# Kernel optimization log

Measured on AMD Instinct MI355X. Metric: run time of the kernel, lower is better.

## Reference

```python
import jax, jax.numpy as jnp
import numpy as np

# Model dims (match init_kwargs)
D_MODEL, D_STATE, D_CONV, EXPAND = 256, 16, 4, 2
D_INNER = EXPAND * D_MODEL           # 512
DT_RANK = (D_MODEL + 15) // 16       # 16
NS_SMALL, NS_BIG = 64, 16
N_BRANCH = 6                         # fwd, bwd, small-slice fwd/bwd, big-slice fwd/bwd
BATCH, SEQLEN = 2, 2048


def setup_inputs() -> dict:
    key = jax.random.key(0)
    ks = jax.random.split(key, 12)
    R2N = DT_RANK + 2 * D_STATE
    # dt_proj bias init as in the module: inverse-softplus of dt ~ LogUniform[1e-3, 1e-1]
    dt = jnp.exp(jax.random.uniform(ks[0], (N_BRANCH, D_INNER)) * (np.log(0.1) - np.log(0.001)) + np.log(0.001))
    dt = jnp.clip(dt, 1e-4, None)
    dt_b = dt + jnp.log(-jnp.expm1(-dt))
    A_log = jnp.log(jnp.broadcast_to(jnp.arange(1, D_STATE + 1, dtype=jnp.float32), (N_BRANCH, D_INNER, D_STATE)))
    return {
        "hidden_states": jax.random.normal(ks[1], (BATCH, SEQLEN, D_MODEL), jnp.float32),
        "in_w": jax.random.normal(ks[2], (2 * D_INNER, D_MODEL), jnp.float32) * (D_MODEL ** -0.5),
        "out_w": jax.random.normal(ks[3], (D_MODEL, D_INNER), jnp.float32) * (D_INNER ** -0.5),
        "conv_w": jax.random.normal(ks[4], (N_BRANCH, D_INNER, D_CONV), jnp.float32) * (D_CONV ** -0.5),
        "conv_b": jax.random.normal(ks[5], (N_BRANCH, D_INNER), jnp.float32) * 0.02,
        "xproj_w": jax.random.normal(ks[6], (N_BRANCH, R2N, D_INNER), jnp.float32) * (D_INNER ** -0.5),
        "dt_w": jax.random.uniform(ks[7], (N_BRANCH, D_INNER, DT_RANK), jnp.float32, -(DT_RANK ** -0.5), DT_RANK ** -0.5),
        "dt_b": dt_b.astype(jnp.float32),
        "A_log": A_log,
        "D_skip": jnp.ones((N_BRANCH, D_INNER), jnp.float32),
    }


def _causal_dwconv(x, w, b):
    # x: (B, D, L); w: (D, K); b: (D,). Causal depthwise conv (torch padding=K-1, keep first L).
    K = w.shape[-1]
    L = x.shape[-1]
    xp = jnp.pad(x, ((0, 0), (0, 0), (K - 1, 0)))
    y = sum(w[:, k][None, :, None] * xp[:, :, k:k + L] for k in range(K))
    return y + b[None, :, None]


def _ssm_scan(delta, u, Bm, Cm, A):
    # delta, u: (B, D, L); Bm, Cm: (B, N, L); A: (D, N) negative reals.
    dT = jnp.moveaxis(delta, -1, 0)  # (L, B, D)
    uT = jnp.moveaxis(u, -1, 0)
    BT = jnp.moveaxis(Bm, -1, 0)     # (L, B, N)
    CT = jnp.moveaxis(Cm, -1, 0)

    def step(h, inp):
        d_t, u_t, b_t, c_t = inp
        dA = jnp.exp(d_t[..., None] * A)                       # (B, D, N)
        h = dA * h + (d_t * u_t)[..., None] * b_t[:, None, :]  # (B, D, N)
        y = jnp.einsum('bdn,bn->bd', h, c_t)
        return h, y

    h0 = jnp.zeros(delta.shape[:2] + (A.shape[-1],), delta.dtype)
    _, ys = jax.lax.scan(step, h0, (dT, uT, BT, CT))
    return jnp.moveaxis(ys, 0, -1)  # (B, D, L)


def _slice_interleave(xz, ns):
    # torch: chunk(ns, dim=-1) -> stack(dim=-1) -> flatten(-2)
    B_, D_, L_ = xz.shape
    return xz.reshape(B_, D_, ns, L_ // ns).swapaxes(-1, -2).reshape(B_, D_, L_)


def _slice_restore(y, ns):
    # torch: reshape(B, D, L//ns, ns).permute(0,1,3,2).flatten(-2)
    B_, D_, L_ = y.shape
    return y.reshape(B_, D_, L_ // ns, ns).swapaxes(-1, -2).reshape(B_, D_, L_)


def reference(hidden_states, in_w, out_w, conv_w, conv_b, xproj_w, dt_w, dt_b, A_log, D_skip):
    R, N = DT_RANK, D_STATE
    xz = jnp.einsum('bld,ed->bel', hidden_states, in_w)  # (B, 2*d_inner, L)

    def branch(xz_i, i):
        x, z = jnp.split(xz_i, 2, axis=1)
        u = jax.nn.silu(_causal_dwconv(x, conv_w[i], conv_b[i]))
        x_dbl = jnp.einsum('bdl,rd->brl', u, xproj_w[i])       # (B, R+2N, L)
        dt_low, Bm, Cm = x_dbl[:, :R], x_dbl[:, R:R + N], x_dbl[:, R + N:]
        delta = jax.nn.softplus(jnp.einsum('brl,dr->bdl', dt_low, dt_w[i]) + dt_b[i][None, :, None])
        A = -jnp.exp(A_log[i])
        y = _ssm_scan(delta, u, Bm, Cm, A) + u * D_skip[i][None, :, None]
        return y * jax.nn.silu(z)

    out = branch(xz, 0)
    out_b = jnp.flip(branch(jnp.flip(xz, -1), 1), -1)
    xz_s = _slice_interleave(xz, NS_SMALL)
    out_s = _slice_restore(branch(xz_s, 2), NS_SMALL)
    out_s_b = _slice_restore(branch(jnp.flip(xz_s, -1), 3), NS_SMALL)
    xz_big = _slice_interleave(xz, NS_BIG)
    out_big = _slice_restore(branch(xz_big, 4), NS_BIG)
    out_big_b = _slice_restore(branch(jnp.flip(xz_big, -1), 5), NS_BIG)

    total = out + out_b + out_s + out_s_b + out_big + out_big_b  # (B, d_inner, L)
    return jnp.einsum('bdl,od->blo', total, out_w)               # (B, L, d_model)
```

## Files before the change

### kernel.cpp

```cpp
#include <hip/hip_runtime.h>
#include <hip/hip_bf16.h>

#define SEQ 2048

typedef __hip_bfloat16 bf16;

__device__ __forceinline__ float silu_f(float x){ return x / (1.f + __expf(-x)); }

__global__ __launch_bounds__(256) void k_ingemm2(const float* __restrict__ hid,
                                                 const float* __restrict__ in_w,
                                                 float* __restrict__ xz,
                                                 const float* __restrict__ xw,
                                                 float* __restrict__ xwT){
    __shared__ float tile[64][65];
    int bid = blockIdx.x;
    if (bid >= 1024) {
        int t = (bid - 1024) * 256 + (int)threadIdx.x;
        int r = t % 48; int dd = (t / 48) % 512; int i = t / (48 * 512);
        xwT[t] = xw[(i * 48 + r) * 512 + dd];
        return;
    }
    int lblk = bid & 31; int eblk = (bid >> 5) & 15; int b = bid >> 9;
    int lane = threadIdx.x & 63;
    int ew = __builtin_amdgcn_readfirstlane((int)threadIdx.x >> 6);
    int l = lblk * 64 + lane;
    int e0 = eblk * 64 + ew * 16;
    int row = threadIdx.x >> 2;
    int c0  = (threadIdx.x & 3) * 16;
    float acc[16];
    #pragma unroll
    for (int k = 0; k < 16; ++k) acc[k] = 0.f;
    for (int dblk = 0; dblk < 4; ++dblk) {
        __syncthreads();
        const float* src = hid + ((size_t)(b * 2048 + lblk * 64 + row)) * 256 + dblk * 64 + c0;
        float4 v0 = *(const float4*)(src + 0);
        float4 v1 = *(const float4*)(src + 4);
        float4 v2 = *(const float4*)(src + 8);
        float4 v3 = *(const float4*)(src + 12);
        tile[row][c0+ 0]=v0.x; tile[row][c0+ 1]=v0.y; tile[row][c0+ 2]=v0.z; tile[row][c0+ 3]=v0.w;
        tile[row][c0+ 4]=v1.x; tile[row][c0+ 5]=v1.y; tile[row][c0+ 6]=v1.z; tile[row][c0+ 7]=v1.w;
        tile[row][c0+ 8]=v2.x; tile[row][c0+ 9]=v2.y; tile[row][c0+10]=v2.z; tile[row][c0+11]=v2.w;
        tile[row][c0+12]=v3.x; tile[row][c0+13]=v3.y; tile[row][c0+14]=v3.z; tile[row][c0+15]=v3.w;
        __syncthreads();
        for (int dd = 0; dd < 64; ++dd) {
            float hv = tile[lane][dd];
            int dg = dblk * 64 + dd;
            #pragma unroll
            for (int k = 0; k < 16; ++k)
                acc[k] = fmaf(in_w[(e0 + k) * 256 + dg], hv, acc[k]);
        }
    }
    #pragma unroll
    for (int k = 0; k < 16; ++k)
        xz[((size_t)(b * 1024 + e0 + k)) * SEQ + l] = acc[k];
}

__global__ __launch_bounds__(256) void k_conv3(const float* __restrict__ xz,
                                               const float* __restrict__ conv_w,
                                               const float* __restrict__ conv_b,
                                               float* __restrict__ u){
    __shared__ float xs[2112];
    int bid = blockIdx.x;
    int d = bid & 511; int b = (bid >> 9) & 1; int p = bid >> 10;
    int sh = (p == 0) ? 11 : (p == 1) ? 6 : 4;
    int mul = SEQ >> sh;
    int inv = 11 - sh;
    const float* xrow = xz + ((size_t)(b * 1024 + d)) * SEQ;
    #pragma unroll
    for (int k = 0; k < 8; ++k) {
        int l = (int)threadIdx.x + k * 256;
        float v = xrow[l];
        int jj = ((l & (mul - 1)) << sh) | (l >> inv);
        xs[jj + (jj >> 5)] = v;
    }
    __syncthreads();
    #pragma unroll
    for (int f = 0; f < 2; ++f) {
        int i = 2 * p + f;
        float w0 = conv_w[(i * 512 + d) * 4 + 0];
        float w1 = conv_w[(i * 512 + d) * 4 + 1];
        float w2 = conv_w[(i * 512 + d) * 4 + 2];
        float w3 = conv_w[(i * 512 + d) * 4 + 3];
        float cb = conv_b[i * 512 + d];
        float* urow = u + ((size_t)((i * 2 + b) * 512 + d)) * SEQ;
        #pragma unroll
        for (int k = 0; k < 8; ++k) {
            int j = (int)threadIdx.x + k * 256;
            float acc = cb;
            #pragma unroll
            for (int m = 0; m < 4; ++m) {
                int idx = j - 3 + m;
                float xv = 0.f;
                if (idx >= 0) {
                    int ridx = f ? (2047 - idx) : idx;
                    xv = xs[ridx + (ridx >> 5)];
                }
                float wm = (m == 0) ? w0 : (m == 1) ? w1 : (m == 2) ? w2 : w3;
                acc = fmaf(wm, xv, acc);
            }
            urow[j] = silu_f(acc);
        }
    }
}

__global__ __launch_bounds__(256) void k_xproj2(const float* __restrict__ u,
                                                const float* __restrict__ xwT,
                                                float* __restrict__ xpart){
    int bid = blockIdx.x;
    int ib = bid % 12; int jt = (bid / 12) % 8; int dq = bid / 96;
    int j = jt * 256 + (int)threadIdx.x;
    int i = ib >> 1;
    const float* ub = u + ((size_t)ib * 512 + dq * 64) * SEQ + j;
    const float* wb = xwT + ((size_t)i * 512 + dq * 64) * 48;
    float acc[48];
    #pragma unroll
    for (int r = 0; r < 48; ++r) acc[r] = 0.f;
    for (int dd = 0; dd < 64; ++dd) {
        float uv = ub[dd * SEQ];
        const float* w = wb + dd * 48;
        #pragma unroll
        for (int r = 0; r < 48; ++r)
            acc[r] = fmaf(w[r], uv, acc[r]);
    }
    float* op = xpart + ((size_t)(dq * 12 + ib) * 48) * SEQ + j;
    #pragma unroll
    for (int r = 0; r < 48; ++r) op[r * SEQ] = acc[r];
}

__global__ __launch_bounds__(256) void k_xbt(const float* __restrict__ xpart,
                                             float* __restrict__ dtlowb,
                                             float* __restrict__ btJ){
    int t = blockIdx.x * 256 + threadIdx.x;
    const int STR = 12 * 48 * SEQ;
    float s = ((xpart[t]           + xpart[t + STR])     + (xpart[t + 2*STR] + xpart[t + 3*STR]))
            + ((xpart[t + 4*STR]   + xpart[t + 5*STR])   + (xpart[t + 6*STR] + xpart[t + 7*STR]));
    int j = t & 2047; int r = (t >> 11) % 48; int ib = t / (48 * 2048);
    if (r < 16) {
        dtlowb[((size_t)(ib * 16 + r)) * 2048 + j] = s;
    } else {
        int q = r - 16; int bc = q >> 4; int n = q & 15; int n2 = n & 3; int k = n >> 2;
        int tt = j & 31; int cc = j >> 5;
        btJ[(((size_t)(ib * 32 + tt) * 64 + cc) << 5) + bc * 16 + n2 * 4 + k] = s;
    }
}

__global__ __launch_bounds__(256, 8) void k_scan(float* __restrict__ u,
                                                 const float* __restrict__ dtlowb,
                                                 const float* __restrict__ btJ,
                                                 const float* __restrict__ dt_w,
                                                 const float* __restrict__ dt_b,
                                                 const float* __restrict__ D_skip){
    __shared__ float sdel[2304];
    __shared__ bf16 sdu[2304];
    __shared__ float sh[1024];
    __shared__ float sS[64];
    int w = blockIdx.x;
    int tid = threadIdx.x;
    int cc = tid >> 2;
    int n2 = tid & 3;
    int d = w & 511; int ib = w >> 9; int i = ib >> 1;
    float Dd = D_skip[i * 512 + d];
    bool s0 = ((n2 + 1) & 1) != 0;
    bool s1 = ((n2 + 1) & 2) != 0;
    bool s2 = ((n2 + 1) & 4) != 0;

    const float4* wv4 = (const float4*)(dt_w + ((size_t)(i * 512 + d)) * 16);
    float4 dw0 = wv4[0], dw1 = wv4[1], dw2 = wv4[2], dw3 = wv4[3];
    float dtb = dt_b[i * 512 + d];

    float4* ug4 = (float4*)(u + (size_t)w * SEQ);
    float4* sd4 = (float4*)sdel;
    __hip_bfloat162* sdu2 = (__hip_bfloat162*)sdu;
    const float4* dtl4 = (const float4*)(dtlowb + (size_t)ib * 16 * 2048);

    float4 ureg0, ureg1;
    #pragma unroll
    for (int part = 0; part < 2; ++part) {
        int jf = tid + part * 256;
        float4 uu = ug4[jf];
        if (part == 0) ureg0 = uu; else ureg1 = uu;
        float4 acc = make_float4(dtb, dtb, dtb, dtb);
        #pragma unroll
        for (int r = 0; r < 16; ++r) {
            float wr = (r < 4)  ? ((r & 3) == 0 ? dw0.x : (r & 3) == 1 ? dw0.y : (r & 3) == 2 ? dw0.z : dw0.w)
                     : (r < 8)  ? ((r & 3) == 0 ? dw1.x : (r & 3) == 1 ? dw1.y : (r & 3) == 2 ? dw1.z : dw1.w)
                     : (r < 12) ? ((r & 3) == 0 ? dw2.x : (r & 3) == 1 ? dw2.y : (r & 3) == 2 ? dw2.z : dw2.w)
                                : ((r & 3) == 0 ? dw3.x : (r & 3) == 1 ? dw3.y : (r & 3) == 2 ? dw3.z : dw3.w);
            float4 q = dtl4[r * 512 + jf];
            acc.x = fmaf(wr, q.x, acc.x);
            acc.y = fmaf(wr, q.y, acc.y);
            acc.z = fmaf(wr, q.z, acc.z);
            acc.w = fmaf(wr, q.w, acc.w);
        }
        float4 Ev, duv;
        {
            float sp = fmaxf(acc.x, 0.f) + __logf(1.f + __expf(-fabsf(acc.x)));
            Ev.x = __expf(-sp); duv.x = sp * uu.x;
            sp = fmaxf(acc.y, 0.f) + __logf(1.f + __expf(-fabsf(acc.y)));
            Ev.y = __expf(-sp); duv.y = sp * uu.y;
            sp = fmaxf(acc.z, 0.f) + __logf(1.f + __expf(-fabsf(acc.z)));
            Ev.z = __expf(-sp); duv.z = sp * uu.z;
            sp = fmaxf(acc.w, 0.f) + __logf(1.f + __expf(-fabsf(acc.w)));
            Ev.w = __expf(-sp); duv.w = sp * uu.w;
        }
        sd4[jf + (jf >> 3)] = Ev;
        int eb = 2 * (jf + (jf >> 3));
        __hip_bfloat162 p0; p0.x = __float2bfloat16(duv.x); p0.y = __float2bfloat16(duv.y);
        __hip_bfloat162 p1; p1.x = __float2bfloat16(duv.z); p1.y = __float2bfloat16(duv.w);
        sdu2[eb]     = p0;
        sdu2[eb + 1] = p1;
    }
    __syncthreads();

    int cbase = cc * 36;
    const float4* bp4 = (const float4*)btJ + ((size_t)ib * 32 * 64 * 8) + cc * 8 + n2;

    float h0 = 0.f, h1 = 0.f, h2 = 0.f, h3 = 0.f, P = 1.f;
    #pragma unroll 4
    for (int tt = 0; tt < 32; ++tt) {
        float E  = sdel[cbase + tt];
        float du = __bfloat162float(sdu[cbase + tt]);
        float4 B = bp4[tt * 512];
        float E2 = E * E, E4 = E2 * E2;
        float e = (s0 ? E : 1.f) * (s1 ? E2 : 1.f) * (s2 ? E4 : 1.f);
        h0 = fmaf(e, h0, du * B.x); e *= E4;
        h1 = fmaf(e, h1, du * B.y); e *= E4;
        h2 = fmaf(e, h2, du * B.z); e *= E4;
        h3 = fmaf(e, h3, du * B.w);
        P *= E;
    }
    sh[cc * 16 + n2]      = h0;
    sh[cc * 16 + n2 + 4]  = h1;
    sh[cc * 16 + n2 + 8]  = h2;
    sh[cc * 16 + n2 + 12] = h3;
    if (n2 == 0) sS[cc] = P;
    __syncthreads();

    if (tid < 16) {
        float hh = 0.f;
        #pragma unroll 4
        for (int c = 0; c < 64; ++c) {
            float Es = sS[c];
            int e = tid + 1;
            float r = 1.f, bsq = Es;
            #pragma unroll
            for (int bit = 0; bit < 5; ++bit) { if (e & 1) r *= bsq; bsq *= bsq; e >>= 1; }
            float tmp = sh[c * 16 + tid];
            sh[c * 16 + tid] = hh;
            hh = fmaf(r, hh, tmp);
        }
    }
    __syncthreads();

    h0 = sh[cc * 16 + n2];
    h1 = sh[cc * 16 + n2 + 4];
    h2 = sh[cc * 16 + n2 + 8];
    h3 = sh[cc * 16 + n2 + 12];
    #pragma unroll 4
    for (int tt = 0; tt < 32; ++tt) {
        float E  = sdel[cbase + tt];
        float du = __bfloat162float(sdu[cbase + tt]);
        float4 B = bp4[tt * 512];
        float4 C = bp4[tt * 512 + 4];
        float E2 = E * E, E4 = E2 * E2;
        float e = (s0 ? E : 1.f) * (s1 ? E2 : 1.f) * (s2 ? E4 : 1.f);
        h0 = fmaf(e, h0, du * B.x); e *= E4;
        h1 = fmaf(e, h1, du * B.y); e *= E4;
        h2 = fmaf(e, h2, du * B.z); e *= E4;
        h3 = fmaf(e, h3, du * B.w);
        float p = h0 * C.x;
        p = fmaf(h1, C.y, p);
        p = fmaf(h2, C.z, p);
        p = fmaf(h3, C.w, p);
        p += __shfl_xor(p, 1, 4);
        p += __shfl_xor(p, 2, 4);
        if (n2 == 0) sdel[cbase + tt] = p;
    }
    __syncthreads();

    {
        int jf = tid;
        float4 y = sd4[jf + (jf >> 3)];
        y.x = fmaf(ureg0.x, Dd, y.x); y.y = fmaf(ureg0.y, Dd, y.y);
        y.z = fmaf(ureg0.z, Dd, y.z); y.w = fmaf(ureg0.w, Dd, y.w);
        ug4[jf] = y;
        jf = tid + 256;
        y = sd4[jf + (jf >> 3)];
        y.x = fmaf(ureg1.x, Dd, y.x); y.y = fmaf(ureg1.y, Dd, y.y);
        y.z = fmaf(ureg1.z, Dd, y.z); y.w = fmaf(ureg1.w, Dd, y.w);
        ug4[jf] = y;
    }
}

__global__ __launch_bounds__(256) void k_gather(const float* __restrict__ y,
                                                const float* __restrict__ xz,
                                                float* __restrict__ total){
    __shared__ bf16 s2[2112], s3[2112], s4[2112], s5[2112];
    int bid = blockIdx.x;
    int d = bid & 511; int b = bid >> 9;
    long base = (long)(b * 512 + d) * SEQ;
    const float* y0 = y + (0 * 1024) * SEQ + base;
    const float* y1 = y + (1 * 1024) * SEQ + base;
    const float* y2r = y + (2 * 1024) * SEQ + base;
    const float* y3r = y + (3 * 1024) * SEQ + base;
    const float* y4r = y + (4 * 1024) * SEQ + base;
    const float* y5r = y + (5 * 1024) * SEQ + base;
    #pragma unroll
    for (int k = 0; k < 8; ++k) {
        int j = (int)threadIdx.x + k * 256;
        int a = j + (j >> 5);
        s2[a] = __float2bfloat16(y2r[j]);
        s3[a] = __float2bfloat16(y3r[j]);
        s4[a] = __float2bfloat16(y4r[j]);
        s5[a] = __float2bfloat16(y5r[j]);
    }
    __syncthreads();
    const float* zrow = xz + (b * 1024 + 512 + d) * SEQ;
    float* trow = total + (b * 512 + d) * SEQ;
    #pragma unroll
    for (int k = 0; k < 8; ++k) {
        int l = (int)threadIdx.x + k * 256;
        int j2 = ((l & 31) << 6) | (l >> 5);
        int j4 = ((l & 127) << 4) | (l >> 7);
        int a2 = j2 + (j2 >> 5);
        int a4 = j4 + (j4 >> 5);
        float s_fwd = y0[l] + y1[2047 - l] + __bfloat162float(s2[a2]) + __bfloat162float(s4[a4]);
        float s_bwd = __bfloat162float(s3[a2]) + __bfloat162float(s5[a4]);
        float zl = silu_f(zrow[l]);
        float zr = silu_f(zrow[2047 - l]);
        trow[l] = fmaf(s_fwd, zl, s_bwd * zr);
    }
}

__global__ __launch_bounds__(256) void k_outgemm(const float* __restrict__ total,
                                                 const float* __restrict__ out_w,
                                                 float* __restrict__ out){
    int lane = threadIdx.x & 63;
    int ow = __builtin_amdgcn_readfirstlane((int)threadIdx.x >> 6);
    int bid = blockIdx.x;
    int lblk = bid & 31; int oblk = (bid >> 5) & 15; int b = bid >> 9;
    int l = lblk * 64 + lane;
    int o0 = oblk * 16 + ow * 4;
    const float* trow = total + b * 512 * SEQ + l;
    float acc[4] = {0,0,0,0};
    for (int d = 0; d < 512; d += 4) {
        float t0 = trow[(d + 0) * SEQ];
        float t1 = trow[(d + 1) * SEQ];
        float t2 = trow[(d + 2) * SEQ];
        float t3 = trow[(d + 3) * SEQ];
        #pragma unroll
        for (int k = 0; k < 4; ++k) {
            float4 wv = *(const float4*)(out_w + (o0 + k) * 512 + d);
            acc[k] = fmaf(wv.x, t0, fmaf(wv.y, t1, fmaf(wv.z, t2, fmaf(wv.w, t3, acc[k]))));
        }
    }
    float* orow = out + ((long)(b * 2048 + l)) * 256 + o0;
    #pragma unroll
    for (int k = 0; k < 4; ++k) orow[k] = acc[k];
}

extern "C" void kernel_launch(void* const* d_in, const int* in_sizes, int n_in,
                              void* d_out, int out_size, void* d_ws, size_t ws_size,
                              hipStream_t stream) {
    const float* hid    = (const float*)d_in[0];
    const float* in_w   = (const float*)d_in[1];
    const float* out_w  = (const float*)d_in[2];
    const float* conv_w = (const float*)d_in[3];
    const float* conv_b = (const float*)d_in[4];
    const float* xw     = (const float*)d_in[5];
    const float* dt_w   = (const float*)d_in[6];
    const float* dt_b   = (const float*)d_in[7];
    const float* D_skip = (const float*)d_in[9];
    float* out = (float*)d_out;

    const size_t off_xz    = 0;
    const size_t off_u     = 4194304;
    const size_t off_xpart = 16777216;
    const size_t off_total = 30539776;
    const size_t need = (size_t)32636928 * 4;
    if (ws_size < need) return;

    float* xz    = (float*)d_ws + off_xz;
    float* u     = (float*)d_ws + off_u;
    float* xpart = (float*)d_ws + off_xpart;
    float* total = (float*)d_ws + off_total;
    float* btJ    = total;
    float* xwT    = total + 786432;
    float* dtlowb = total + 933888;

    k_ingemm2 <<<1600, 256, 0, stream>>>(hid, in_w, xz, xw, xwT);
    k_conv3   <<<3072, 256, 0, stream>>>(xz, conv_w, conv_b, u);
    k_xproj2  <<<768,  256, 0, stream>>>(u, xwT, xpart);
    k_xbt     <<<4608, 256, 0, stream>>>(xpart, dtlowb, btJ);
    k_scan    <<<6144, 256, 0, stream>>>(u, dtlowb, btJ, dt_w, dt_b, D_skip);
    k_gather  <<<1024, 256, 0, stream>>>(u, xz, total);
    k_outgemm <<<1024, 256, 0, stream>>>(total, out_w, out);
}
```

Measured before the change: 384.4 us.

## Fuse x-projection split-K reduction into projection kernel and restructure chunked scan

Merges the x-projection and its separate split-K reduction kernel into one kernel that reduces partial sums in shared memory and writes dt_low and the B/C layout directly. This removes the large xpart round trip through global memory and one launch. The scan is reorganised into 128 chunks of 16 steps with 8 states per thread, a two-level parallel carry propagation and a new B/C layout, with occupancy hint lowered to 7. Only 384 blocks now run the projection, so parallelism there drops.

Result: slower. 754.0 us (+96.1%).

```diff
diff --git a/kernel.cpp b/kernel.cpp
--- a/kernel.cpp
+++ b/kernel.cpp
@@ -103,73 +103,87 @@
     }
 }
 
-__global__ __launch_bounds__(256) void k_xproj2(const float* __restrict__ u,
+__global__ __launch_bounds__(256) void k_xproj3(const float* __restrict__ u,
                                                 const float* __restrict__ xwT,
-                                                float* __restrict__ xpart){
+                                                float* __restrict__ dtlowb,
+                                                float* __restrict__ btJ){
+    __shared__ __align__(16) float sred[12288];
     int bid = blockIdx.x;
-    int ib = bid % 12; int jt = (bid / 12) % 8; int dq = bid / 96;
-    int j = jt * 256 + (int)threadIdx.x;
-    int i = ib >> 1;
-    const float* ub = u + ((size_t)ib * 512 + dq * 64) * SEQ + j;
-    const float* wb = xwT + ((size_t)i * 512 + dq * 64) * 48;
+    int jt = bid & 31; int ib = bid >> 5; int i = ib >> 1;
+    int tid = (int)threadIdx.x;
+    int j = tid & 63;
+    int ks = __builtin_amdgcn_readfirstlane(tid >> 6);
+    int j0 = jt * 64;
+    const float* ub = u + ((size_t)(ib * 512 + ks * 128)) * SEQ + j0 + j;
+    const float* wb = xwT + ((size_t)(i * 512 + ks * 128)) * 48;
     float acc[48];
     #pragma unroll
     for (int r = 0; r < 48; ++r) acc[r] = 0.f;
-    for (int dd = 0; dd < 64; ++dd) {
-        float uv = ub[dd * SEQ];
-        const float* w = wb + dd * 48;
-        #pragma unroll
-        for (int r = 0; r < 48; ++r)
-            acc[r] = fmaf(w[r], uv, acc[r]);
-    }
-    float* op = xpart + ((size_t)(dq * 12 + ib) * 48) * SEQ + j;
-    #pragma unroll
-    for (int r = 0; r < 48; ++r) op[r * SEQ] = acc[r];
-}
-
-__global__ __launch_bounds__(256) void k_xbt(const float* __restrict__ xpart,
-                                             float* __restrict__ dtlowb,
-                                             float* __restrict__ btJ){
-    int t = blockIdx.x * 256 + threadIdx.x;
-    const int STR = 12 * 48 * SEQ;
-    float s = ((xpart[t]           + xpart[t + STR])     + (xpart[t + 2*STR] + xpart[t + 3*STR]))
-            + ((xpart[t + 4*STR]   + xpart[t + 5*STR])   + (xpart[t + 6*STR] + xpart[t + 7*STR]));
-    int j = t & 2047; int r = (t >> 11) % 48; int ib = t / (48 * 2048);
-    if (r < 16) {
-        dtlowb[((size_t)(ib * 16 + r)) * 2048 + j] = s;
-    } else {
-        int q = r - 16; int bc = q >> 4; int n = q & 15; int n2 = n & 3; int k = n >> 2;
-        int tt = j & 31; int cc = j >> 5;
-        btJ[(((size_t)(ib * 32 + tt) * 64 + cc) << 5) + bc * 16 + n2 * 4 + k] = s;
-    }
-}
-
-__global__ __launch_bounds__(256, 8) void k_scan(float* __restrict__ u,
+    #pragma unroll 4
+    for (int dd = 0; dd < 128; ++dd) {
+        float uv = ub[(size_t)dd * SEQ];
+        const float* ww = wb + dd * 48;
+        #pragma unroll
+        for (int r = 0; r < 48; ++r) acc[r] = fmaf(ww[r], uv, acc[r]);
+    }
+    #pragma unroll
+    for (int r = 0; r < 48; ++r) sred[r * 256 + tid] = acc[r];
+    __syncthreads();
+    const float4* sred4 = (const float4*)sred;
+    {
+        int rr = tid >> 4; int j4 = tid & 15;
+        float4 a0 = sred4[rr * 64 +  0 + j4];
+        float4 a1 = sred4[rr * 64 + 16 + j4];
+        float4 a2 = sred4[rr * 64 + 32 + j4];
+        float4 a3 = sred4[rr * 64 + 48 + j4];
+        float4 s;
+        s.x = (a0.x + a1.x) + (a2.x + a3.x);
+        s.y = (a0.y + a1.y) + (a2.y + a3.y);
+        s.z = (a0.z + a1.z) + (a2.z + a3.z);
+        s.w = (a0.w + a1.w) + (a2.w + a3.w);
+        ((float4*)(dtlowb + ((size_t)(ib * 16 + rr)) * SEQ + j0))[j4] = s;
+    }
+    {
+        int sel = tid >> 5; int n2 = sel & 1; int mq = (sel >> 1) & 1; int bc = sel >> 2;
+        int jb = tid & 31;
+        #pragma unroll
+        for (int half = 0; half < 2; ++half) {
+            int jj = jb + half * 32;
+            int jg = j0 + jj; int cc = jg >> 4; int tt = jg & 15;
+            float4 v;
+            #pragma unroll
+            for (int mm = 0; mm < 4; ++mm) {
+                int row = 16 + bc * 16 + n2 + 8 * mq + 2 * mm;
+                const float* rp = sred + row * 256 + jj;
+                float s = (rp[0] + rp[64]) + (rp[128] + rp[192]);
+                (&v.x)[mm] = s;
+            }
+            ((float4*)btJ)[((((size_t)(ib * 128 + cc) * 2 + n2) * 2 + bc) * 2 + mq) * 16 + tt] = v;
+        }
+    }
+}
+
+__global__ __launch_bounds__(256, 7) void k_scan(float* __restrict__ u,
                                                  const float* __restrict__ dtlowb,
                                                  const float* __restrict__ btJ,
                                                  const float* __restrict__ dt_w,
                                                  const float* __restrict__ dt_b,
                                                  const float* __restrict__ D_skip){
-    __shared__ float sdel[2304];
-    __shared__ bf16 sdu[2304];
-    __shared__ float sh[1024];
-    __shared__ float sS[64];
+    __shared__ __align__(16) float sdel[2560];
+    __shared__ __align__(16) bf16  sdu[2048];
+    __shared__ __align__(16) float shh[2048];
+    __shared__ float sS[128];
     int w = blockIdx.x;
-    int tid = threadIdx.x;
-    int cc = tid >> 2;
-    int n2 = tid & 3;
+    int tid = (int)threadIdx.x;
     int d = w & 511; int ib = w >> 9; int i = ib >> 1;
     float Dd = D_skip[i * 512 + d];
-    bool s0 = ((n2 + 1) & 1) != 0;
-    bool s1 = ((n2 + 1) & 2) != 0;
-    bool s2 = ((n2 + 1) & 4) != 0;
 
     const float4* wv4 = (const float4*)(dt_w + ((size_t)(i * 512 + d)) * 16);
     float4 dw0 = wv4[0], dw1 = wv4[1], dw2 = wv4[2], dw3 = wv4[3];
     float dtb = dt_b[i * 512 + d];
 
     float4* ug4 = (float4*)(u + (size_t)w * SEQ);
-    float4* sd4 = (float4*)sdel;
+    float4* sdel4 = (float4*)sdel;
     __hip_bfloat162* sdu2 = (__hip_bfloat162*)sdu;
     const float4* dtl4 = (const float4*)(dtlowb + (size_t)ib * 16 * 2048);
 
@@ -203,92 +217,145 @@
             sp = fmaxf(acc.w, 0.f) + __logf(1.f + __expf(-fabsf(acc.w)));
             Ev.w = __expf(-sp); duv.w = sp * uu.w;
         }
-        sd4[jf + (jf >> 3)] = Ev;
-        int eb = 2 * (jf + (jf >> 3));
+        int ccw = jf >> 2; int tq = jf & 3;
+        sdel4[ccw * 5 + tq] = Ev;
         __hip_bfloat162 p0; p0.x = __float2bfloat16(duv.x); p0.y = __float2bfloat16(duv.y);
         __hip_bfloat162 p1; p1.x = __float2bfloat16(duv.z); p1.y = __float2bfloat16(duv.w);
-        sdu2[eb]     = p0;
-        sdu2[eb + 1] = p1;
-    }
-    __syncthreads();
-
-    int cbase = cc * 36;
-    const float4* bp4 = (const float4*)btJ + ((size_t)ib * 32 * 64 * 8) + cc * 8 + n2;
-
-    float h0 = 0.f, h1 = 0.f, h2 = 0.f, h3 = 0.f, P = 1.f;
-    #pragma unroll 4
-    for (int tt = 0; tt < 32; ++tt) {
-        float E  = sdel[cbase + tt];
-        float du = __bfloat162float(sdu[cbase + tt]);
-        float4 B = bp4[tt * 512];
-        float E2 = E * E, E4 = E2 * E2;
-        float e = (s0 ? E : 1.f) * (s1 ? E2 : 1.f) * (s2 ? E4 : 1.f);
-        h0 = fmaf(e, h0, du * B.x); e *= E4;
-        h1 = fmaf(e, h1, du * B.y); e *= E4;
-        h2 = fmaf(e, h2, du * B.z); e *= E4;
-        h3 = fmaf(e, h3, du * B.w);
-        P *= E;
-    }
-    sh[cc * 16 + n2]      = h0;
-    sh[cc * 16 + n2 + 4]  = h1;
-    sh[cc * 16 + n2 + 8]  = h2;
-    sh[cc * 16 + n2 + 12] = h3;
-    if (n2 == 0) sS[cc] = P;
-    __syncthreads();
-
-    if (tid < 16) {
-        float hh = 0.f;
-        #pragma unroll 4
-        for (int c = 0; c < 64; ++c) {
-            float Es = sS[c];
-            int e = tid + 1;
-            float r = 1.f, bsq = Es;
+        sdu2[ccw * 8 + tq * 2]     = p0;
+        sdu2[ccw * 8 + tq * 2 + 1] = p1;
+    }
+    __syncthreads();
+
+    int cc = tid >> 1; int n2 = tid & 1;
+    const float4* bt4 = (const float4*)btJ + ((size_t)((ib * 128 + cc) * 2 + n2)) * 64;
+    const uint2* sduq = (const uint2*)sdu;
+
+    float h0=0.f,h1=0.f,h2=0.f,h3=0.f,h4=0.f,h5=0.f,h6=0.f,h7=0.f;
+    float P = 1.f;
+    #pragma unroll
+    for (int tg = 0; tg < 4; ++tg) {
+        float4 Ev = sdel4[cc * 5 + tg];
+        uint2 dz = sduq[cc * 4 + tg];
+        #pragma unroll
+        for (int q = 0; q < 4; ++q) {
+            int tt = tg * 4 + q;
+            float E = (&Ev.x)[q];
+            unsigned ubits = (q < 2) ? dz.x : dz.y;
+            float du = __uint_as_float((q & 1) ? (ubits & 0xffff0000u) : (ubits << 16));
+            float4 B0 = bt4[tt];
+            float4 B1 = bt4[16 + tt];
+            float E2 = E * E;
+            float e = n2 ? E2 : E;
+            h0 = fmaf(e, h0, du * B0.x); e *= E2;
+            h1 = fmaf(e, h1, du * B0.y); e *= E2;
+            h2 = fmaf(e, h2, du * B0.z); e *= E2;
+            h3 = fmaf(e, h3, du * B0.w); e *= E2;
+            h4 = fmaf(e, h4, du * B1.x); e *= E2;
+            h5 = fmaf(e, h5, du * B1.y); e *= E2;
+            h6 = fmaf(e, h6, du * B1.z); e *= E2;
+            h7 = fmaf(e, h7, du * B1.w);
+            P *= E;
+        }
+    }
+    {
+        int sb = cc * 16 + n2;
+        shh[sb]      = h0; shh[sb + 2]  = h1; shh[sb + 4]  = h2; shh[sb + 6]  = h3;
+        shh[sb + 8]  = h4; shh[sb + 10] = h5; shh[sb + 12] = h6; shh[sb + 14] = h7;
+        if (n2 == 0) sS[cc] = P;
+    }
+    __syncthreads();
+
+    if (tid < 64) {
+        int n = tid & 15; int cg = tid >> 4;
+        int e = n + 1;
+        int c0 = cg * 32;
+        float Rs[32];
+        float A = 1.f, Bv = 0.f;
+        #pragma unroll
+        for (int q = 0; q < 32; ++q) {
+            float Pc = sS[c0 + q];
+            float r = 1.f, s = Pc; int ee = e;
             #pragma unroll
-            for (int bit = 0; bit < 5; ++bit) { if (e & 1) r *= bsq; bsq *= bsq; e >>= 1; }
-            float tmp = sh[c * 16 + tid];
-            sh[c * 16 + tid] = hh;
-            hh = fmaf(r, hh, tmp);
-        }
-    }
-    __syncthreads();
-
-    h0 = sh[cc * 16 + n2];
-    h1 = sh[cc * 16 + n2 + 4];
-    h2 = sh[cc * 16 + n2 + 8];
-    h3 = sh[cc * 16 + n2 + 12];
-    #pragma unroll 4
-    for (int tt = 0; tt < 32; ++tt) {
-        float E  = sdel[cbase + tt];
-        float du = __bfloat162float(sdu[cbase + tt]);
-        float4 B = bp4[tt * 512];
-        float4 C = bp4[tt * 512 + 4];
-        float E2 = E * E, E4 = E2 * E2;
-        float e = (s0 ? E : 1.f) * (s1 ? E2 : 1.f) * (s2 ? E4 : 1.f);
-        h0 = fmaf(e, h0, du * B.x); e *= E4;
-        h1 = fmaf(e, h1, du * B.y); e *= E4;
-        h2 = fmaf(e, h2, du * B.z); e *= E4;
-        h3 = fmaf(e, h3, du * B.w);
-        float p = h0 * C.x;
-        p = fmaf(h1, C.y, p);
-        p = fmaf(h2, C.z, p);
-        p = fmaf(h3, C.w, p);
-        p += __shfl_xor(p, 1, 4);
-        p += __shfl_xor(p, 2, 4);
-        if (n2 == 0) sdel[cbase + tt] = p;
+            for (int bit = 0; bit < 5; ++bit) { if (ee & 1) r *= s; s *= s; ee >>= 1; }
+            Rs[q] = r;
+            float L = shh[(c0 + q) * 16 + n];
+            A *= r;
+            Bv = fmaf(r, Bv, L);
+        }
+        float H = 0.f;
+        #pragma unroll
+        for (int k = 0; k < 3; ++k) {
+            float a = __shfl(A, k * 16 + n);
+            float b = __shfl(Bv, k * 16 + n);
+            if (cg > k) H = fmaf(a, H, b);
+        }
+        float hc = H;
+        #pragma unroll
+        for (int q = 0; q < 32; ++q) {
+            int sidx = (c0 + q) * 16 + n;
+            float tmp = shh[sidx];
+            shh[sidx] = hc;
+            hc = fmaf(Rs[q], hc, tmp);
+        }
+    }
+    __syncthreads();
+
+    {
+        int sb = cc * 16 + n2;
+        h0 = shh[sb];      h1 = shh[sb + 2];  h2 = shh[sb + 4];  h3 = shh[sb + 6];
+        h4 = shh[sb + 8];  h5 = shh[sb + 10]; h6 = shh[sb + 12]; h7 = shh[sb + 14];
+    }
+    #pragma unroll
+    for (int tg = 0; tg < 4; ++tg) {
+        float4 Ev = sdel4[cc * 5 + tg];
+        uint2 dz = sduq[cc * 4 + tg];
+        float4 yv;
+        #pragma unroll
+        for (int q = 0; q < 4; ++q) {
+            int tt = tg * 4 + q;
+            float E = (&Ev.x)[q];
+            unsigned ubits = (q < 2) ? dz.x : dz.y;
+            float du = __uint_as_float((q & 1) ? (ubits & 0xffff0000u) : (ubits << 16));
+            float4 B0 = bt4[tt];
+            float4 B1 = bt4[16 + tt];
+            float4 C0 = bt4[32 + tt];
+            float4 C1 = bt4[48 + tt];
+            float E2 = E * E;
+            float e = n2 ? E2 : E;
+            h0 = fmaf(e, h0, du * B0.x); e *= E2;
+            h1 = fmaf(e, h1, du * B0.y); e *= E2;
+            h2 = fmaf(e, h2, du * B0.z); e *= E2;
+            h3 = fmaf(e, h3, du * B0.w); e *= E2;
+            h4 = fmaf(e, h4, du * B1.x); e *= E2;
+            h5 = fmaf(e, h5, du * B1.y); e *= E2;
+            h6 = fmaf(e, h6, du * B1.z); e *= E2;
+            h7 = fmaf(e, h7, du * B1.w);
+            float p = h0 * C0.x;
+            p = fmaf(h1, C0.y, p);
+            p = fmaf(h2, C0.z, p);
+            p = fmaf(h3, C0.w, p);
+            p = fmaf(h4, C1.x, p);
+            p = fmaf(h5, C1.y, p);
+            p = fmaf(h6, C1.z, p);
+            p = fmaf(h7, C1.w, p);
+            p += __shfl_xor(p, 1, 2);
+            (&yv.x)[q] = p;
+        }
+        if (n2 == 0) sdel4[cc * 5 + tg] = yv;
     }
     __syncthreads();
 
     {
         int jf = tid;
-        float4 y = sd4[jf + (jf >> 3)];
+        float4 y = sdel4[(jf >> 2) * 5 + (jf & 3)];
         y.x = fmaf(ureg0.x, Dd, y.x); y.y = fmaf(ureg0.y, Dd, y.y);
         y.z = fmaf(ureg0.z, Dd, y.z); y.w = fmaf(ureg0.w, Dd, y.w);
         ug4[jf] = y;
         jf = tid + 256;
-        y = sd4[jf + (jf >> 3)];
-        y.x = fmaf(ureg1.x, Dd, y.x); y.y = fmaf(ureg1.y, Dd, y.y);
-        y.z = fmaf(ureg1.z, Dd, y.z); y.w = fmaf(ureg1.w, Dd, y.w);
-        ug4[jf] = y;
+        float4 y2 = sdel4[(jf >> 2) * 5 + (jf & 3)];
+        y2.x = fmaf(ureg1.x, Dd, y2.x); y2.y = fmaf(ureg1.y, Dd, y2.y);
+        y2.z = fmaf(ureg1.z, Dd, y2.z); y2.w = fmaf(ureg1.w, Dd, y2.w);
+        ug4[jf] = y2;
     }
 }
 
@@ -375,14 +442,12 @@
 
     const size_t off_xz    = 0;
     const size_t off_u     = 4194304;
-    const size_t off_xpart = 16777216;
     const size_t off_total = 30539776;
     const size_t need = (size_t)32636928 * 4;
     if (ws_size < need) return;
 
     float* xz    = (float*)d_ws + off_xz;
     float* u     = (float*)d_ws + off_u;
-    float* xpart = (float*)d_ws + off_xpart;
     float* total = (float*)d_ws + off_total;
     float* btJ    = total;
     float* xwT    = total + 786432;
@@ -390,8 +455,7 @@
 
     k_ingemm2 <<<1600, 256, 0, stream>>>(hid, in_w, xz, xw, xwT);
     k_conv3   <<<3072, 256, 0, stream>>>(xz, conv_w, conv_b, u);
-    k_xproj2  <<<768,  256, 0, stream>>>(u, xwT, xpart);
-    k_xbt     <<<4608, 256, 0, stream>>>(xpart, dtlowb, btJ);
+    k_xproj3  <<<384,  256, 0, stream>>>(u, xwT, dtlowb, btJ);
     k_scan    <<<6144, 256, 0, stream>>>(u, dtlowb, btJ, dt_w, dt_b, D_skip);
     k_gather  <<<1024, 256, 0, stream>>>(u, xz, total);
     k_outgemm <<<1024, 256, 0, stream>>>(total, out_w, out);
```

## Fuse x_proj split-K reduction into projection kernel via shared memory

Applied to the files above, without the earlier changes.

Merges the x_proj partial GEMM and the separate split-K reduction/scatter kernel into one kernel. Each block splits the 512-channel reduction across four wavefronts, reduces the partials in shared memory, and writes dt_low and the reordered B/C layout directly. This removes the round trip of eight partial result planes through global memory and one kernel launch. In exchange it launches fewer blocks (384 instead of 768) with a large 48 KB shared buffer, which lowers parallelism and occupancy.

New measurement: 385.9 us. No clear change (+0.4%).

```diff
diff --git a/kernel.cpp b/kernel.cpp
--- a/kernel.cpp
+++ b/kernel.cpp
@@ -103,44 +103,65 @@
     }
 }
 
-__global__ __launch_bounds__(256) void k_xproj2(const float* __restrict__ u,
+__global__ __launch_bounds__(256) void k_xproj3(const float* __restrict__ u,
                                                 const float* __restrict__ xwT,
-                                                float* __restrict__ xpart){
+                                                float* __restrict__ dtlowb,
+                                                float* __restrict__ btJ){
+    __shared__ __align__(16) float sred[12288];
     int bid = blockIdx.x;
-    int ib = bid % 12; int jt = (bid / 12) % 8; int dq = bid / 96;
-    int j = jt * 256 + (int)threadIdx.x;
-    int i = ib >> 1;
-    const float* ub = u + ((size_t)ib * 512 + dq * 64) * SEQ + j;
-    const float* wb = xwT + ((size_t)i * 512 + dq * 64) * 48;
+    int jt = bid & 31; int ib = bid >> 5; int i = ib >> 1;
+    int tid = (int)threadIdx.x;
+    int j = tid & 63;
+    int ks = __builtin_amdgcn_readfirstlane(tid >> 6);
+    int j0 = jt * 64;
+    const float* ub = u + ((size_t)(ib * 512 + ks * 128)) * SEQ + j0 + j;
+    const float* wb = xwT + ((size_t)(i * 512 + ks * 128)) * 48;
     float acc[48];
     #pragma unroll
     for (int r = 0; r < 48; ++r) acc[r] = 0.f;
-    for (int dd = 0; dd < 64; ++dd) {
-        float uv = ub[dd * SEQ];
-        const float* w = wb + dd * 48;
+    #pragma unroll 4
+    for (int dd = 0; dd < 128; ++dd) {
+        float uv = ub[(size_t)dd * SEQ];
+        const float* ww = wb + dd * 48;
         #pragma unroll
-        for (int r = 0; r < 48; ++r)
-            acc[r] = fmaf(w[r], uv, acc[r]);
-    }
-    float* op = xpart + ((size_t)(dq * 12 + ib) * 48) * SEQ + j;
-    #pragma unroll
-    for (int r = 0; r < 48; ++r) op[r * SEQ] = acc[r];
-}
-
-__global__ __launch_bounds__(256) void k_xbt(const float* __restrict__ xpart,
-                                             float* __restrict__ dtlowb,
-                                             float* __restrict__ btJ){
-    int t = blockIdx.x * 256 + threadIdx.x;
-    const int STR = 12 * 48 * SEQ;
-    float s = ((xpart[t]           + xpart[t + STR])     + (xpart[t + 2*STR] + xpart[t + 3*STR]))
-            + ((xpart[t + 4*STR]   + xpart[t + 5*STR])   + (xpart[t + 6*STR] + xpart[t + 7*STR]));
-    int j = t & 2047; int r = (t >> 11) % 48; int ib = t / (48 * 2048);
-    if (r < 16) {
-        dtlowb[((size_t)(ib * 16 + r)) * 2048 + j] = s;
-    } else {
-        int q = r - 16; int bc = q >> 4; int n = q & 15; int n2 = n & 3; int k = n >> 2;
-        int tt = j & 31; int cc = j >> 5;
-        btJ[(((size_t)(ib * 32 + tt) * 64 + cc) << 5) + bc * 16 + n2 * 4 + k] = s;
+        for (int r = 0; r < 48; ++r) acc[r] = fmaf(ww[r], uv, acc[r]);
+    }
+    #pragma unroll
+    for (int r = 0; r < 48; ++r) sred[r * 256 + tid] = acc[r];
+    __syncthreads();
+    const float4* sred4 = (const float4*)sred;
+    {
+        int rr = tid >> 4; int j4 = tid & 15;
+        float4 a0 = sred4[rr * 64 +  0 + j4];
+        float4 a1 = sred4[rr * 64 + 16 + j4];
+        float4 a2 = sred4[rr * 64 + 32 + j4];
+        float4 a3 = sred4[rr * 64 + 48 + j4];
+        float4 s;
+        s.x = (a0.x + a1.x) + (a2.x + a3.x);
+        s.y = (a0.y + a1.y) + (a2.y + a3.y);
+        s.z = (a0.z + a1.z) + (a2.z + a3.z);
+        s.w = (a0.w + a1.w) + (a2.w + a3.w);
+        ((float4*)(dtlowb + ((size_t)(ib * 16 + rr)) * SEQ + j0))[j4] = s;
+    }
+    {
+        int sel = tid >> 5; int bc = sel >> 2; int n2q = sel & 3;
+        int jb = tid & 31;
+        #pragma unroll
+        for (int half = 0; half < 2; ++half) {
+            int jj = jb + half * 32;
+            int jg = j0 + jj; int cc0 = jg >> 5; int tt0 = jg & 31;
+            int row0 = 16 + bc * 16 + n2q;
+            const float* rp0 = sred + (row0 + 0)  * 256 + jj;
+            const float* rp1 = sred + (row0 + 4)  * 256 + jj;
+            const float* rp2 = sred + (row0 + 8)  * 256 + jj;
+            const float* rp3 = sred + (row0 + 12) * 256 + jj;
+            float4 v;
+            v.x = (rp0[0] + rp0[64]) + (rp0[128] + rp0[192]);
+            v.y = (rp1[0] + rp1[64]) + (rp1[128] + rp1[192]);
+            v.z = (rp2[0] + rp2[64]) + (rp2[128] + rp2[192]);
+            v.w = (rp3[0] + rp3[64]) + (rp3[128] + rp3[192]);
+            ((float4*)btJ)[(size_t)ib * 16384 + (size_t)tt0 * 512 + cc0 * 8 + bc * 4 + n2q] = v;
+        }
     }
 }
 
@@ -375,14 +396,12 @@
 
     const size_t off_xz    = 0;
     const size_t off_u     = 4194304;
-    const size_t off_xpart = 16777216;
     const size_t off_total = 30539776;
     const size_t need = (size_t)32636928 * 4;
     if (ws_size < need) return;
 
     float* xz    = (float*)d_ws + off_xz;
     float* u     = (float*)d_ws + off_u;
-    float* xpart = (float*)d_ws + off_xpart;
     float* total = (float*)d_ws + off_total;
     float* btJ    = total;
     float* xwT    = total + 786432;
@@ -390,8 +409,7 @@
 
     k_ingemm2 <<<1600, 256, 0, stream>>>(hid, in_w, xz, xw, xwT);
     k_conv3   <<<3072, 256, 0, stream>>>(xz, conv_w, conv_b, u);
-    k_xproj2  <<<768,  256, 0, stream>>>(u, xwT, xpart);
-    k_xbt     <<<4608, 256, 0, stream>>>(xpart, dtlowb, btJ);
+    k_xproj3  <<<384,  256, 0, stream>>>(u, xwT, dtlowb, btJ);
     k_scan    <<<6144, 256, 0, stream>>>(u, dtlowb, btJ, dt_w, dt_b, D_skip);
     k_gather  <<<1024, 256, 0, stream>>>(u, xz, total);
     k_outgemm <<<1024, 256, 0, stream>>>(total, out_w, out);
```
